# Kernel tuning notes

Measured on AMD Instinct MI355X. Metric: run time of the kernel, lower is better.

The kernel has to match this reference:

```python
import jax, jax.numpy as jnp
import numpy as np

B, N, P, D, H = 16, 256, 8, 512, 8
E = P * D  # 4096, flattened patch embedding width


def _sincos_pos_embed(q_len, d_model):
    # PatchTST-style 'sincos' positional encoding (learn_pe=False buffer)
    pe = np.zeros((q_len, d_model), dtype=np.float64)
    position = np.arange(q_len, dtype=np.float64)[:, None]
    div_term = np.exp(np.arange(0, d_model, 2, dtype=np.float64) * -(np.log(10000.0) / d_model))
    pe[:, 0::2] = np.sin(position * div_term)
    pe[:, 1::2] = np.cos(position * div_term)
    pe = pe - pe.mean()
    pe = pe / (pe.std() * 10)
    return jnp.asarray(pe, dtype=jnp.float32)


def setup_inputs() -> dict:
    key = jax.random.key(0)
    ks = jax.random.split(key, 10)
    s = 0.02
    return {
        "x": jax.random.normal(ks[0], (B, N, P, D), dtype=jnp.float32),
        "pos_embed": _sincos_pos_embed(N, E),
        "W_embed": jax.random.normal(ks[1], (E, E), dtype=jnp.float32) * s,
        "b_embed": jnp.zeros((E,), dtype=jnp.float32),
        "Wq": jax.random.normal(ks[2], (E, E), dtype=jnp.float32) * s,
        "bq": jnp.zeros((E,), dtype=jnp.float32),
        "Wk": jax.random.normal(ks[3], (E, E), dtype=jnp.float32) * s,
        "bk": jnp.zeros((E,), dtype=jnp.float32),
        "Wv": jax.random.normal(ks[4], (E, E), dtype=jnp.float32) * s,
        "bv": jnp.zeros((E,), dtype=jnp.float32),
        "Wo": jax.random.normal(ks[5], (E, E), dtype=jnp.float32) * s,
        "bo": jnp.zeros((E,), dtype=jnp.float32),
    }


def reference(x, pos_embed, W_embed, b_embed, Wq, bq, Wk, bk, Wv, bv, Wo, bo):
    b, n, p, d = x.shape
    h = H
    dh = E // h  # per-head dim = patch_size * d_keys
    xe = x.reshape(b, n, p * d)                       # B N (P D)
    xe = xe @ W_embed.T + b_embed                     # embed_linear
    xe = xe + pos_embed                               # pos embed (dropout=0, eval)
    q = (xe @ Wq.T + bq).reshape(b, n, h, dh)
    k = (xe @ Wk.T + bk).reshape(b, n, h, dh)
    v = (xe @ Wv.T + bv).reshape(b, n, h, dh)
    scale = 1.0 / np.sqrt(d // h)                     # NOTE: uses d_model//H, not E//H (faithful)
    attn_scores = jnp.einsum('bnhd,bmhd->bhnm', q, k) * scale
    attn_weights = jax.nn.softmax(attn_scores, axis=-1)
    out = jnp.einsum('bhnm,bmhd->bnhd', attn_weights, v).reshape(b, n, h * dh)
    out = out @ Wo.T + bo
    out = out.reshape(b, n, p, d)
    return out, attn_weights
```

## Files before the change

### kernel.cpp

```cpp
#include <hip/hip_runtime.h>
#include <hip/hip_bf16.h>


typedef unsigned short u16;
typedef _Float16 f16;
typedef __attribute__((ext_vector_type(8))) _Float16 v8h;
typedef __attribute__((ext_vector_type(8))) short vu16x8;
typedef __attribute__((ext_vector_type(4))) float vf32x4;

#define MFMA_F16(a, b, c) __builtin_amdgcn_mfma_f32_16x16x32_f16(a, b, c, 0, 0, 0)

__device__ __forceinline__ void gld16(const void* g, void* l) {
    __builtin_amdgcn_global_load_lds((const __attribute__((address_space(1))) void*)g,
                                     (__attribute__((address_space(3))) void*)l,
                                     16, 0, 0);
}

__global__ __launch_bounds__(256) void tof16(const float* __restrict__ s,
                                             f16* __restrict__ d) {
    const size_t i = ((size_t)blockIdx.x * 256 + threadIdx.x) * 4;
    const float4 v = *(const float4*)(s + i);
    d[i + 0] = (f16)v.x; d[i + 1] = (f16)v.y;
    d[i + 2] = (f16)v.z; d[i + 3] = (f16)v.w;
}

template <int MODE>
__global__ __launch_bounds__(512, 4)
void gemm4_nt(const f16* __restrict__ A, const f16* __restrict__ Bw,
              const float* __restrict__ bias, const f16* __restrict__ posh,
              f16* __restrict__ Ch, float* __restrict__ Cf) {
    __shared__ __align__(16) u16 sA[16384];
    __shared__ __align__(16) u16 sB[8192];
    const int t = threadIdx.x;
    const int lane = t & 63, w = t >> 6;
    const int wm = w >> 1, wn = w & 1;
    const int l15 = lane & 15, lg = lane >> 4;
    const int wg = ((blockIdx.x & 7) << 6) + (blockIdx.x >> 3);
    const int m0 = (wg >> 5) << 8, n0 = (wg & 31) << 7;

    int aRow[4], aCol[4], bRow[2], bCol[2];
#pragma unroll
    for (int i = 0; i < 4; ++i) {
        const int c = t + (i << 9);
        aRow[i] = c >> 3;
        aCol[i] = (((c & 7) ^ (aRow[i] & 7)) << 3);
    }
#pragma unroll
    for (int i = 0; i < 2; ++i) {
        const int c = t + (i << 9);
        bRow[i] = c >> 3;
        bCol[i] = (((c & 7) ^ (bRow[i] & 7)) << 3);
    }
    const int rA = (wm << 6) + l15;
    const int rB = (wn << 6) + l15;
    const int xA = rA & 7, xB = rB & 7;

    vf32x4 acc[4][4] = {};

    for (int kt = 0; kt < 64; ++kt) {
        const int k0 = kt << 6;
#pragma unroll
        for (int i = 0; i < 4; ++i) {
            const int c = t + (i << 9);
            gld16(A + (((size_t)(m0 + aRow[i])) << 12) + k0 + aCol[i],
                  &sA[c * 8]);
        }
#pragma unroll
        for (int i = 0; i < 2; ++i) {
            const int c = t + (i << 9);
            gld16(Bw + (((size_t)(n0 + bRow[i])) << 12) + k0 + bCol[i],
                  &sB[c * 8]);
        }
        asm volatile("s_waitcnt vmcnt(0)" ::: "memory");
        __builtin_amdgcn_s_barrier();
        asm volatile("" ::: "memory");
#pragma unroll
        for (int kk = 0; kk < 2; ++kk) {
            const int ccA = (((kk << 2) + lg) ^ xA) << 3;
            const int ccB = (((kk << 2) + lg) ^ xB) << 3;
            v8h av[4], bv[4];
#pragma unroll
            for (int m = 0; m < 4; ++m)
                av[m] = *(const v8h*)(&sA[(rA << 6) + (m << 10) + ccA]);
#pragma unroll
            for (int n = 0; n < 4; ++n)
                bv[n] = *(const v8h*)(&sB[(rB << 6) + (n << 10) + ccB]);
            asm volatile("s_waitcnt lgkmcnt(0)" ::: "memory");
            __builtin_amdgcn_sched_barrier(0);
            __builtin_amdgcn_s_setprio(1);
#pragma unroll
            for (int m = 0; m < 4; ++m)
#pragma unroll
                for (int n = 0; n < 4; ++n)
                    acc[m][n] = MFMA_F16(av[m], bv[n], acc[m][n]);
            __builtin_amdgcn_s_setprio(0);
        }
        __builtin_amdgcn_s_barrier();
        asm volatile("" ::: "memory");
    }

#pragma unroll
    for (int n = 0; n < 4; ++n) {
        const int col = n0 + (wn << 6) + (n << 4) + l15;
        const float bvv = bias[col];
#pragma unroll
        for (int m = 0; m < 4; ++m) {
#pragma unroll
            for (int r = 0; r < 4; ++r) {
                const int row = m0 + (wm << 6) + (m << 4) + (lg << 2) + r;
                float v = acc[m][n][r] + bvv;
                if (MODE == 0)
                    v += (float)posh[((size_t)(row & 255) << 12) + col];
                if (MODE == 2)
                    Cf[((size_t)row << 12) + col] = v;
                else
                    Ch[((size_t)row << 12) + col] = (f16)v;
            }
        }
    }
}

__global__ __launch_bounds__(256)
void attn_scores(const f16* __restrict__ q, const f16* __restrict__ k,
                 float* __restrict__ Pf, f16* __restrict__ Pb) {
    const int blk = ((blockIdx.x & 7) << 6) + (blockIdx.x >> 3);
    const int bh = blk >> 2, it = blk & 3;
    const int b = bh >> 3, h = bh & 7;
    const size_t qoff = ((size_t)(b * 256 + it * 64) << 12) + (h << 9);
    const size_t koff = ((size_t)(b * 256) << 12) + (h << 9);
    __shared__ __align__(16) u16 Qs[64 * 64];
    __shared__ __align__(16) u16 Ks[256 * 64];
    __shared__ float red[4][64];

    const int t = threadIdx.x;
    const int lane = t & 63, w = t >> 6;
    const int l15 = lane & 15, lg = lane >> 4;

    vf32x4 acc[4][4] = {};

    for (int k0 = 0; k0 < 512; k0 += 64) {
#pragma unroll
        for (int i = 0; i < 2; ++i) {
            const int c = t + (i << 8);
            const int row = c >> 3, c8 = (c & 7) << 3;
            gld16(q + qoff + ((size_t)row << 12) + k0 + c8, Qs + c * 8);
        }
#pragma unroll
        for (int i = 0; i < 8; ++i) {
            const int c = t + (i << 8);
            const int row = c >> 3, c8 = (c & 7) << 3;
            gld16(k + koff + ((size_t)row << 12) + k0 + c8, Ks + c * 8);
        }
        __syncthreads();
#pragma unroll
        for (int kk = 0; kk < 2; ++kk) {
            v8h af[4], bf[4];
#pragma unroll
            for (int m = 0; m < 4; ++m)
                af[m] = *(const v8h*)(Qs + (m * 16 + l15) * 64 + kk * 32 + lg * 8);
#pragma unroll
            for (int n = 0; n < 4; ++n)
                bf[n] = *(const v8h*)(Ks + (w * 64 + n * 16 + l15) * 64 + kk * 32 + lg * 8);
#pragma unroll
            for (int m = 0; m < 4; ++m)
#pragma unroll
                for (int n = 0; n < 4; ++n)
                    acc[m][n] = MFMA_F16(af[m], bf[n], acc[m][n]);
        }
        __syncthreads();
    }

#pragma unroll
    for (int m = 0; m < 4; ++m)
#pragma unroll
        for (int n = 0; n < 4; ++n) acc[m][n] *= 0.125f;

    float gm[4][4];
#pragma unroll
    for (int m = 0; m < 4; ++m)
#pragma unroll
        for (int r = 0; r < 4; ++r) {
            float v = fmaxf(fmaxf(acc[m][0][r], acc[m][1][r]),
                            fmaxf(acc[m][2][r], acc[m][3][r]));
#pragma unroll
            for (int off = 1; off < 16; off <<= 1) v = fmaxf(v, __shfl_xor(v, off));
            gm[m][r] = v;
        }
    if (l15 == 0) {
#pragma unroll
        for (int m = 0; m < 4; ++m)
#pragma unroll
            for (int r = 0; r < 4; ++r) red[w][m * 16 + lg * 4 + r] = gm[m][r];
    }
    __syncthreads();
#pragma unroll
    for (int m = 0; m < 4; ++m)
#pragma unroll
        for (int r = 0; r < 4; ++r) {
            const int row = m * 16 + lg * 4 + r;
            gm[m][r] = fmaxf(fmaxf(red[0][row], red[1][row]),
                             fmaxf(red[2][row], red[3][row]));
        }
    __syncthreads();

    float gs[4][4];
#pragma unroll
    for (int m = 0; m < 4; ++m)
#pragma unroll
        for (int r = 0; r < 4; ++r) {
            float s = 0.f;
#pragma unroll
            for (int n = 0; n < 4; ++n) {
                const float e = __expf(acc[m][n][r] - gm[m][r]);
                acc[m][n][r] = e;
                s += e;
            }
#pragma unroll
            for (int off = 1; off < 16; off <<= 1) s += __shfl_xor(s, off);
            gs[m][r] = s;
        }
    if (l15 == 0) {
#pragma unroll
        for (int m = 0; m < 4; ++m)
#pragma unroll
            for (int r = 0; r < 4; ++r) red[w][m * 16 + lg * 4 + r] = gs[m][r];
    }
    __syncthreads();

    const size_t pbase = ((size_t)bh * 256 + it * 64) * 256;
#pragma unroll
    for (int m = 0; m < 4; ++m)
#pragma unroll
        for (int r = 0; r < 4; ++r) {
            const int row = m * 16 + lg * 4 + r;
            const float inv = 1.0f / (red[0][row] + red[1][row] +
                                      red[2][row] + red[3][row]);
#pragma unroll
            for (int n = 0; n < 4; ++n) {
                const int col = w * 64 + n * 16 + l15;
                const float p = acc[m][n][r] * inv;
                Pf[pbase + (size_t)row * 256 + col] = p;
                Pb[pbase + (size_t)row * 256 + col] = (f16)p;
            }
        }
}

__global__ __launch_bounds__(256)
void attn_pv(const f16* __restrict__ P, const f16* __restrict__ V,
             f16* __restrict__ O) {
    __shared__ __align__(16) u16 Ps[128 * 64];
    __shared__ __align__(16) u16 Vt[128 * 72];
    const int t = threadIdx.x;
    const int lane = t & 63, w = t >> 6;
    const int wr = (w >> 1) << 6, wc = (w & 1) << 6;
    const int l15 = lane & 15, lg = lane >> 4;
    const int blk = ((blockIdx.x & 7) << 7) + (blockIdx.x >> 3);
    const int bh = blk >> 3, mt = (blk >> 2) & 1, nt = blk & 3;
    const int b = bh >> 3, h = bh & 7;
    const f16* Pbp = P + ((size_t)bh << 16) + ((size_t)mt << 15);
    const u16* Vb = (const u16*)V + ((size_t)(b * 256) << 12) + (h << 9) + (nt << 7);

    vf32x4 acc[4][4] = {};

    for (int k0 = 0; k0 < 256; k0 += 64) {
#pragma unroll
        for (int i = 0; i < 4; ++i) {
            const int c = t + (i << 8);
            const int row = c >> 3, c8 = (c & 7) << 3;
            gld16(Pbp + (size_t)row * 256 + k0 + c8, Ps + c * 8);
        }
#pragma unroll
        for (int pp = 0; pp < 4; ++pp) {
            const int kr = pp * 16 + (t >> 4);
            const int c8 = (t & 15) << 3;
            vu16x8 vv = *(const vu16x8*)(Vb + ((size_t)(k0 + kr) << 12) + c8);
#pragma unroll
            for (int c = 0; c < 8; ++c) Vt[(c8 + c) * 72 + kr] = (u16)vv[c];
        }
        __syncthreads();
#pragma unroll
        for (int kk = 0; kk < 2; ++kk) {
            v8h af[4], bf[4];
#pragma unroll
            for (int m = 0; m < 4; ++m)
                af[m] = *(const v8h*)(Ps + (wr + m * 16 + l15) * 64 + kk * 32 + lg * 8);
#pragma unroll
            for (int n = 0; n < 4; ++n)
                bf[n] = *(const v8h*)(Vt + (wc + n * 16 + l15) * 72 + kk * 32 + lg * 8);
#pragma unroll
            for (int m = 0; m < 4; ++m)
#pragma unroll
                for (int n = 0; n < 4; ++n)
                    acc[m][n] = MFMA_F16(af[m], bf[n], acc[m][n]);
        }
        __syncthreads();
    }

#pragma unroll
    for (int m = 0; m < 4; ++m)
#pragma unroll
        for (int n = 0; n < 4; ++n) {
            const int col = (h << 9) + (nt << 7) + wc + n * 16 + l15;
#pragma unroll
            for (int r = 0; r < 4; ++r) {
                const int row = b * 256 + mt * 128 + wr + m * 16 + lg * 4 + r;
                O[((size_t)row << 12) + col] = (f16)acc[m][n][r];
            }
        }
}

extern "C" void kernel_launch(void* const* d_in, const int* in_sizes, int n_in,
                              void* d_out, int out_size, void* d_ws, size_t ws_size,
                              hipStream_t stream) {
    const float* x   = (const float*)d_in[0];
    const float* pos = (const float*)d_in[1];
    const float* wE  = (const float*)d_in[2];
    const float* bE  = (const float*)d_in[3];
    const float* wQ  = (const float*)d_in[4];
    const float* bq  = (const float*)d_in[5];
    const float* wK  = (const float*)d_in[6];
    const float* bk  = (const float*)d_in[7];
    const float* wV  = (const float*)d_in[8];
    const float* bv  = (const float*)d_in[9];
    const float* wO  = (const float*)d_in[10];
    const float* bo  = (const float*)d_in[11];

    float* out  = (float*)d_out;
    float* Pout = out + (size_t)16777216;

    char* W = (char*)d_ws;
    const size_t MB = 1024 * 1024;
    f16* xf    = (f16*)(W + 0 * MB);
    f16* wslab = (f16*)(W + 32 * MB);
    f16* xe    = (f16*)(W + 64 * MB);
    f16* qs    = (f16*)(W + 96 * MB);
    f16* ks    = (f16*)(W + 128 * MB);
    f16* vs    = (f16*)(W + 160 * MB);
    f16* Pb    = (f16*)(W + 192 * MB);
    f16* posh  = (f16*)(W + 208 * MB);
    f16* ao    = xf;

    const int CVG = 16384;
    const int CVP = 1024;

    tof16<<<CVP, 256, 0, stream>>>(pos, posh);
    tof16<<<CVG, 256, 0, stream>>>(x, xf);
    tof16<<<CVG, 256, 0, stream>>>(wE, wslab);
    gemm4_nt<0><<<512, 512, 0, stream>>>(xf, wslab, bE, posh, xe, nullptr);

    tof16<<<CVG, 256, 0, stream>>>(wQ, wslab);
    gemm4_nt<1><<<512, 512, 0, stream>>>(xe, wslab, bq, nullptr, qs, nullptr);

    tof16<<<CVG, 256, 0, stream>>>(wK, wslab);
    gemm4_nt<1><<<512, 512, 0, stream>>>(xe, wslab, bk, nullptr, ks, nullptr);

    tof16<<<CVG, 256, 0, stream>>>(wV, wslab);
    gemm4_nt<1><<<512, 512, 0, stream>>>(xe, wslab, bv, nullptr, vs, nullptr);

    attn_scores<<<512, 256, 0, stream>>>(qs, ks, Pout, Pb);
    attn_pv<<<1024, 256, 0, stream>>>(Pb, vs, ao);

    tof16<<<CVG, 256, 0, stream>>>(wO, wslab);
    gemm4_nt<2><<<512, 512, 0, stream>>>(ao, wslab, bo, nullptr, nullptr, out);
}
```

Before: 811.2 us.

## Fuse Q, K, V projections into one concatenated-weight GEMM launch

Converts Wq, Wk and Wv into one contiguous f16 weight slab and runs a single GEMM over 1536 workgroups with 256x128 tiles, writing Q, K and V into adjacent buffers. This replaces three separate GEMM launches and lets xe tiles be reused across all three projections, which should also improve wave fill. The new kernel loads A and B tiles without double buffering, and the workspace is re-laid out so posh, the weight slab and Pb share the same region.

```diff
diff --git a/kernel.cpp b/kernel.cpp
--- a/kernel.cpp
+++ b/kernel.cpp
@@ -115,6 +115,100 @@
                     Cf[((size_t)row << 12) + col] = v;
                 else
                     Ch[((size_t)row << 12) + col] = (f16)v;
+            }
+        }
+    }
+}
+
+__global__ __launch_bounds__(512, 4)
+void gemmqkv_nt(const f16* __restrict__ A, const f16* __restrict__ Wc,
+                const float* __restrict__ bq, const float* __restrict__ bk,
+                const float* __restrict__ bv_, f16* __restrict__ qkv) {
+    __shared__ __align__(16) u16 sA[16384];
+    __shared__ __align__(16) u16 sB[8192];
+    const int t = threadIdx.x;
+    const int lane = t & 63, w = t >> 6;
+    const int wm = w >> 1, wn = w & 1;
+    const int l15 = lane & 15, lg = lane >> 4;
+    const int wg = ((blockIdx.x & 7) * 192) + (blockIdx.x >> 3);
+    const int m0 = (wg / 96) << 8;
+    const int nglob = (wg % 96) << 7;
+    const int which = nglob >> 12;
+    const int n0 = nglob & 4095;
+    const float* bias = (which == 0) ? bq : (which == 1) ? bk : bv_;
+    f16* Ch = qkv + ((size_t)which << 24);
+
+    int aRow[4], aCol[4], bRow[2], bCol[2];
+#pragma unroll
+    for (int i = 0; i < 4; ++i) {
+        const int c = t + (i << 9);
+        aRow[i] = c >> 3;
+        aCol[i] = (((c & 7) ^ (aRow[i] & 7)) << 3);
+    }
+#pragma unroll
+    for (int i = 0; i < 2; ++i) {
+        const int c = t + (i << 9);
+        bRow[i] = c >> 3;
+        bCol[i] = (((c & 7) ^ (bRow[i] & 7)) << 3);
+    }
+    const int rA = (wm << 6) + l15;
+    const int rB = (wn << 6) + l15;
+    const int xA = rA & 7, xB = rB & 7;
+
+    vf32x4 acc[4][4] = {};
+
+    for (int kt = 0; kt < 64; ++kt) {
+        const int k0 = kt << 6;
+#pragma unroll
+        for (int i = 0; i < 4; ++i) {
+            const int c = t + (i << 9);
+            gld16(A + (((size_t)(m0 + aRow[i])) << 12) + k0 + aCol[i],
+                  &sA[c * 8]);
+        }
+#pragma unroll
+        for (int i = 0; i < 2; ++i) {
+            const int c = t + (i << 9);
+            gld16(Wc + (((size_t)(nglob + bRow[i])) << 12) + k0 + bCol[i],
+                  &sB[c * 8]);
+        }
+        asm volatile("s_waitcnt vmcnt(0)" ::: "memory");
+        __builtin_amdgcn_s_barrier();
+        asm volatile("" ::: "memory");
+#pragma unroll
+        for (int kk = 0; kk < 2; ++kk) {
+            const int ccA = (((kk << 2) + lg) ^ xA) << 3;
+            const int ccB = (((kk << 2) + lg) ^ xB) << 3;
+            v8h av[4], bv[4];
+#pragma unroll
+            for (int m = 0; m < 4; ++m)
+                av[m] = *(const v8h*)(&sA[(rA << 6) + (m << 10) + ccA]);
+#pragma unroll
+            for (int n = 0; n < 4; ++n)
+                bv[n] = *(const v8h*)(&sB[(rB << 6) + (n << 10) + ccB]);
+            asm volatile("s_waitcnt lgkmcnt(0)" ::: "memory");
+            __builtin_amdgcn_sched_barrier(0);
+            __builtin_amdgcn_s_setprio(1);
+#pragma unroll
+            for (int m = 0; m < 4; ++m)
+#pragma unroll
+                for (int n = 0; n < 4; ++n)
+                    acc[m][n] = MFMA_F16(av[m], bv[n], acc[m][n]);
+            __builtin_amdgcn_s_setprio(0);
+        }
+        __builtin_amdgcn_s_barrier();
+        asm volatile("" ::: "memory");
+    }
+
+#pragma unroll
+    for (int n = 0; n < 4; ++n) {
+        const int col = n0 + (wn << 6) + (n << 4) + l15;
+        const float bvv = bias[col];
+#pragma unroll
+        for (int m = 0; m < 4; ++m) {
+#pragma unroll
+            for (int r = 0; r < 4; ++r) {
+                const int row = m0 + (wm << 6) + (m << 4) + (lg << 2) + r;
+                Ch[((size_t)row << 12) + col] = (f16)(acc[m][n][r] + bvv);
             }
         }
     }
@@ -333,11 +427,13 @@
     f16* xf    = (f16*)(W + 0 * MB);
     f16* wslab = (f16*)(W + 32 * MB);
     f16* xe    = (f16*)(W + 64 * MB);
-    f16* qs    = (f16*)(W + 96 * MB);
-    f16* ks    = (f16*)(W + 128 * MB);
-    f16* vs    = (f16*)(W + 160 * MB);
-    f16* Pb    = (f16*)(W + 192 * MB);
-    f16* posh  = (f16*)(W + 208 * MB);
+    f16* posh  = (f16*)(W + 96 * MB);
+    f16* wqkv  = (f16*)(W + 96 * MB);
+    f16* Pb    = (f16*)(W + 96 * MB);
+    f16* qkv   = (f16*)(W + 192 * MB);
+    f16* qs    = qkv;
+    f16* ks    = qkv + (size_t)16777216;
+    f16* vs    = qkv + (size_t)33554432;
     f16* ao    = xf;
 
     const int CVG = 16384;
@@ -348,14 +444,10 @@
     tof16<<<CVG, 256, 0, stream>>>(wE, wslab);
     gemm4_nt<0><<<512, 512, 0, stream>>>(xf, wslab, bE, posh, xe, nullptr);
 
-    tof16<<<CVG, 256, 0, stream>>>(wQ, wslab);
-    gemm4_nt<1><<<512, 512, 0, stream>>>(xe, wslab, bq, nullptr, qs, nullptr);
-
-    tof16<<<CVG, 256, 0, stream>>>(wK, wslab);
-    gemm4_nt<1><<<512, 512, 0, stream>>>(xe, wslab, bk, nullptr, ks, nullptr);
-
-    tof16<<<CVG, 256, 0, stream>>>(wV, wslab);
-    gemm4_nt<1><<<512, 512, 0, stream>>>(xe, wslab, bv, nullptr, vs, nullptr);
+    tof16<<<CVG, 256, 0, stream>>>(wQ, wqkv);
+    tof16<<<CVG, 256, 0, stream>>>(wK, wqkv + (size_t)16777216);
+    tof16<<<CVG, 256, 0, stream>>>(wV, wqkv + (size_t)33554432);
+    gemmqkv_nt<<<1536, 512, 0, stream>>>(xe, wqkv, bq, bk, bv, qkv);
 
     attn_scores<<<512, 256, 0, stream>>>(qs, ks, Pout, Pb);
     attn_pv<<<1024, 256, 0, stream>>>(Pb, vs, ao);
```

Result: slower. 847.8 us (+4.5%).
